# Optimization experiments

Measured on AMD Instinct MI355X. Metric: run time of the kernel, lower is better.

## Reference

```python
import jax, jax.numpy as jnp
import numpy as np

D_MODEL, D_K, D_V, N_HEADS = 1024, 64, 64, 16
B, S = 4, 4096
LN_EPS = 1e-5
NORM_EPS = 1e-12  # torch F.normalize default eps


def setup_inputs() -> dict:
    key = jax.random.key(0)
    ks = jax.random.split(key, 9)
    s = 0.02
    return {
        "x": jax.random.normal(ks[0], (B, S, D_MODEL), dtype=jnp.float32),
        # nn.Linear weights have shape [out, in]
        "W_Q": jax.random.normal(ks[1], (N_HEADS * D_K, D_MODEL), dtype=jnp.float32) * s,
        "W_K": jax.random.normal(ks[2], (N_HEADS * D_K, D_MODEL), dtype=jnp.float32) * s,
        "W_V": jax.random.normal(ks[3], (N_HEADS * D_V, D_MODEL), dtype=jnp.float32) * s,
        "W_g": jax.random.normal(ks[4], (N_HEADS * D_V, D_MODEL), dtype=jnp.float32) * s,
        "W_alpha": jax.random.normal(ks[5], (N_HEADS, D_MODEL), dtype=jnp.float32) * s,
        "W_O": jax.random.normal(ks[6], (D_MODEL, N_HEADS * D_V), dtype=jnp.float32) * s,
        "ln_gamma": jnp.ones((D_MODEL,), dtype=jnp.float32),
        "ln_beta": jnp.zeros((D_MODEL,), dtype=jnp.float32),
    }


def reference(x, W_Q, W_K, W_V, W_g, W_alpha, W_O, ln_gamma, ln_beta):
    # --- input projection chain (unfused variant) ---
    Q_raw = jnp.einsum('bsd,od->bso', x, W_Q)               # [B,S,H*Dk] (unused downstream)
    K_raw = jnp.einsum('bsd,od->bso', x, W_K)               # [B,S,H*Dk]
    V = jnp.einsum('bsd,od->bso', x, W_V)                   # [B,S,H*Dv]
    g_raw = jnp.einsum('bsd,od->bso', x, W_g)               # [B,S,H*Dv]
    alpha_raw = jnp.einsum('bsd,od->bso', x, W_alpha)       # [B,S,H]

    # F.normalize over the full last dim (n_heads*d_k), eps clamp on the norm
    K_norm = K_raw / jnp.maximum(jnp.linalg.norm(K_raw, axis=-1, keepdims=True), NORM_EPS)
    gate = jax.nn.silu(g_raw)
    alpha = jax.nn.sigmoid(alpha_raw)

    # scan is simulated as identity: scan_output = V
    scan_output = V

    # --- output epilogue: gate-multiply + output GEMM + residual + LayerNorm ---
    gated = scan_output * gate
    projected = jnp.einsum('bsv,dv->bsd', gated, W_O)
    pre = projected + x
    mean = jnp.mean(pre, axis=-1, keepdims=True)
    var = jnp.mean(jnp.square(pre - mean), axis=-1, keepdims=True)
    out = (pre - mean) * jax.lax.rsqrt(var + LN_EPS) * ln_gamma + ln_beta
    return out
```

## Files before the change

### kernel.cpp

```cpp
#include <hip/hip_runtime.h>

#define M_TOT 16384
#define DM    1024

typedef unsigned short ushort_t;
typedef __bf16 bf16x8 __attribute__((ext_vector_type(8)));
typedef float  f32x4  __attribute__((ext_vector_type(4)));

__device__ __forceinline__ ushort_t f32_to_bf16(float f) {
    union { float f; unsigned u; } v; v.f = f;
    unsigned u = v.u;
    return (ushort_t)((u + 0x7fffu + ((u >> 16) & 1u)) >> 16);
}
__device__ __forceinline__ float bf16_to_f32(ushort_t h) {
    union { unsigned u; float f; } v; v.u = ((unsigned)h) << 16;
    return v.f;
}

__device__ __forceinline__ void gload16(const ushort_t* g, ushort_t* l) {
    __builtin_amdgcn_global_load_lds(
        (const __attribute__((address_space(1))) unsigned int*)g,
        (__attribute__((address_space(3))) unsigned int*)l,
        16, 0, 0);
}

__global__ __launch_bounds__(256) void cvt_all(const float* __restrict__ x,
                                               const float* __restrict__ wv,
                                               const float* __restrict__ wg,
                                               const float* __restrict__ wo,
                                               ushort_t* __restrict__ xb,
                                               ushort_t* __restrict__ wcat,
                                               ushort_t* __restrict__ wob) {
    const long NX = (long)M_TOT * DM / 4, NW = (long)DM * DM / 4;
    long i = (long)blockIdx.x * 256 + threadIdx.x;
    const float* src; ushort_t* dst; long so, di;
    if (i < NX) {
        src = x; so = i; dst = xb; di = i;
    } else if (i < NX + NW) {
        long j = i - NX; src = wv; so = j;
        int row = (int)(j >> 8), c4 = (int)(j & 255);
        int orow = ((row >> 4) << 5) | (row & 15);
        dst = wcat; di = (long)orow * 256 + c4;
    } else if (i < NX + 2 * NW) {
        long j = i - NX - NW; src = wg; so = j;
        int row = (int)(j >> 8), c4 = (int)(j & 255);
        int orow = ((row >> 4) << 5) | 16 | (row & 15);
        dst = wcat; di = (long)orow * 256 + c4;
    } else {
        long j = i - NX - 2 * NW; src = wo; so = j; dst = wob; di = j;
    }
    const float4 v = ((const float4*)src)[so];
    ushort4 o;
    o.x = f32_to_bf16(v.x); o.y = f32_to_bf16(v.y);
    o.z = f32_to_bf16(v.z); o.w = f32_to_bf16(v.w);
    ((ushort4*)dst)[di] = o;
}

template<int EPI>
__global__ __launch_bounds__(512, 2) void gemmS(
    const ushort_t* __restrict__ A,
    const ushort_t* __restrict__ Bm,
    const ushort_t* __restrict__ Xb,
    ushort_t* __restrict__ out,
    int nbs)
{
    extern __shared__ ushort_t lds[];

    const int flat = blockIdx.x;
    const int xcd  = flat & 7;
    const int ii   = flat >> 3;
    const int m0   = ((xcd << 3) + (ii >> nbs)) << 8;
    const int n0   = (ii & ((1 << nbs) - 1)) << 8;

    const int tid  = threadIdx.x;
    const int w    = tid >> 6;
    const int l    = tid & 63;
    const int wm   = w >> 2;
    const int wn   = w & 3;
    const int fr   = l & 15;
    const int quad = l >> 4;

    f32x4 acc[8][4];
    const f32x4 vzero = {0.f, 0.f, 0.f, 0.f};
#pragma unroll
    for (int i = 0; i < 8; ++i)
#pragma unroll
        for (int j = 0; j < 4; ++j) acc[i][j] = vzero;

    const long sA0 = (long)(m0 + w * 16 + fr) * DM + (quad << 3);
    const long sA1 = sA0 + 128 * (long)DM;
    const long sB0 = (long)(n0 + w * 16 + fr) * DM + (quad << 3);
    const long sB1 = sB0 + 128 * (long)DM;

    auto stageA = [&](int u) {
        const int d  = (u & 3) * 16384 + w * 512;
        const int ko = u * 32;
        gload16(A + sA0 + ko, lds + d);
        gload16(A + sA1 + ko, lds + d + 4096);
    };
    auto stageB = [&](int u) {
        const int d  = (u & 3) * 16384 + 8192 + w * 512;
        const int ko = u * 32;
        gload16(Bm + sB0 + ko, lds + d);
        gload16(Bm + sB1 + ko, lds + d + 4096);
    };

    const int rA = wm * 4096 + l * 8;
    const int rB = 8192 + wn * 2048 + l * 8;

    stageA(0); stageB(0);
    stageA(1); stageB(1);
    stageA(2); stageB(2);
    asm volatile("s_waitcnt vmcnt(8)" ::: "memory");
    __builtin_amdgcn_s_barrier();

    for (int u = 0; u < 32; ++u) {
        const int sb = (u & 3) * 16384;
        bf16x8 af[4], bf[4];

#pragma unroll
        for (int j = 0; j < 4; ++j) bf[j] = *(const bf16x8*)(lds + sb + rB + j * 512);
#pragma unroll
        for (int i = 0; i < 4; ++i) af[i] = *(const bf16x8*)(lds + sb + rA + i * 512);
        if (u < 29) stageA(u + 3);
        __builtin_amdgcn_s_barrier();
        __builtin_amdgcn_s_setprio(1);
#pragma unroll
        for (int j = 0; j < 4; ++j)
#pragma unroll
            for (int i = 0; i < 4; ++i)
                acc[i][j] = __builtin_amdgcn_mfma_f32_16x16x32_bf16(
                    af[i], bf[j], acc[i][j], 0, 0, 0);
        __builtin_amdgcn_s_setprio(0);
        __builtin_amdgcn_s_barrier();

#pragma unroll
        for (int i = 0; i < 4; ++i) af[i] = *(const bf16x8*)(lds + sb + rA + (4 + i) * 512);
        if (u < 29) stageB(u + 3);
        __builtin_amdgcn_s_barrier();
        __builtin_amdgcn_s_setprio(1);
#pragma unroll
        for (int j = 0; j < 4; ++j)
#pragma unroll
            for (int i = 0; i < 4; ++i)
                acc[4 + i][j] = __builtin_amdgcn_mfma_f32_16x16x32_bf16(
                    af[i], bf[j], acc[4 + i][j], 0, 0, 0);
        __builtin_amdgcn_s_setprio(0);
        if (u < 29)       { asm volatile("s_waitcnt vmcnt(8)" ::: "memory"); }
        else if (u == 29) { asm volatile("s_waitcnt vmcnt(4)" ::: "memory"); }
        else if (u == 30) { asm volatile("s_waitcnt vmcnt(0)" ::: "memory"); }
        __builtin_amdgcn_sched_barrier(0);
        __builtin_amdgcn_s_barrier();
    }

    const int rowb = m0 + wm * 128;
    const int colb = n0 + wn * 64;
    if (EPI == 0) {
#pragma unroll
        for (int i = 0; i < 8; ++i)
#pragma unroll
            for (int jp = 0; jp < 2; ++jp) {
                const int cb   = colb + jp * 32;
                const int vcol = ((cb >> 5) << 4) + fr;
#pragma unroll
                for (int r = 0; r < 4; ++r) {
                    const int row = rowb + i * 16 + quad * 4 + r;
                    float v = acc[i][2 * jp][r];
                    float g = acc[i][2 * jp + 1][r];
                    float gate = g / (1.0f + __expf(-g));
                    out[(long)row * DM + vcol] = f32_to_bf16(v * gate);
                }
            }
    } else {
#pragma unroll
        for (int i = 0; i < 8; ++i)
#pragma unroll
            for (int j = 0; j < 4; ++j) {
                const int col = colb + j * 16 + fr;
#pragma unroll
                for (int r = 0; r < 4; ++r) {
                    const int row = rowb + i * 16 + quad * 4 + r;
                    float pre = acc[i][j][r] + bf16_to_f32(Xb[(long)row * DM + col]);
                    out[(long)row * DM + col] = f32_to_bf16(pre);
                }
            }
    }
}

__global__ __launch_bounds__(256) void ln_rows(const ushort_t* __restrict__ pre,
                                               const float* __restrict__ gamma,
                                               const float* __restrict__ beta,
                                               float* __restrict__ out)
{
    const int row = blockIdx.x;
    const int tid = threadIdx.x;
    const int wave = tid >> 6, lane = tid & 63;

    ushort4 u = ((const ushort4*)(pre + row * DM))[tid];
    float p0 = bf16_to_f32(u.x), p1 = bf16_to_f32(u.y);
    float p2 = bf16_to_f32(u.z), p3 = bf16_to_f32(u.w);

    float s  = p0 + p1 + p2 + p3;
    float ss = p0 * p0 + p1 * p1 + p2 * p2 + p3 * p3;
#pragma unroll
    for (int off = 32; off > 0; off >>= 1) {
        s  += __shfl_down(s, off);
        ss += __shfl_down(ss, off);
    }
    __shared__ float red[8];
    __shared__ float mb[2];
    if (lane == 0) { red[wave] = s; red[4 + wave] = ss; }
    __syncthreads();
    if (tid == 0) {
        float S  = red[0] + red[1] + red[2] + red[3];
        float SS = red[4] + red[5] + red[6] + red[7];
        float mean = S * (1.0f / 1024.0f);
        float var  = SS * (1.0f / 1024.0f) - mean * mean;
        mb[0] = mean;
        mb[1] = rsqrtf(var + 1e-5f);
    }
    __syncthreads();
    const float mean = mb[0], rs = mb[1];

    float4 gm = ((const float4*)gamma)[tid];
    float4 bt = ((const float4*)beta)[tid];
    float4 o;
    o.x = (p0 - mean) * rs * gm.x + bt.x;
    o.y = (p1 - mean) * rs * gm.y + bt.y;
    o.z = (p2 - mean) * rs * gm.z + bt.z;
    o.w = (p3 - mean) * rs * gm.w + bt.w;
    ((float4*)(out + row * DM))[tid] = o;
}

extern "C" void kernel_launch(void* const* d_in, const int* in_sizes, int n_in,
                              void* d_out, int out_size, void* d_ws, size_t ws_size,
                              hipStream_t stream) {
    const float* x     = (const float*)d_in[0];
    const float* WV    = (const float*)d_in[3];
    const float* WG    = (const float*)d_in[4];
    const float* WO    = (const float*)d_in[6];
    const float* gamma = (const float*)d_in[7];
    const float* beta  = (const float*)d_in[8];
    float* out = (float*)d_out;

    char* ws = (char*)d_ws;
    ushort_t* xb    = (ushort_t*)ws;
    ushort_t* gated = (ushort_t*)(ws + (size_t)M_TOT * DM * 2);
    ushort_t* wcat  = (ushort_t*)(ws + (size_t)M_TOT * DM * 4);
    ushort_t* wob   = (ushort_t*)(ws + (size_t)M_TOT * DM * 4 + (size_t)2 * DM * DM * 2);
    ushort_t* pre   = xb;

    static bool attr_set = false;
    if (!attr_set) {
        hipFuncSetAttribute((const void*)&gemmS<0>,
                            hipFuncAttributeMaxDynamicSharedMemorySize, 131072);
        hipFuncSetAttribute((const void*)&gemmS<1>,
                            hipFuncAttributeMaxDynamicSharedMemorySize, 131072);
        attr_set = true;
    }

    const int nCvt = (M_TOT * DM + 3 * DM * DM) / 4 / 256;
    cvt_all<<<nCvt, 256, 0, stream>>>(x, WV, WG, WO, xb, wcat, wob);

    gemmS<0><<<512, 512, 131072, stream>>>(xb, wcat, nullptr, gated, 3);
    gemmS<1><<<256, 512, 131072, stream>>>(gated, wob, xb, pre, 2);

    ln_rows<<<M_TOT, 256, 0, stream>>>(pre, gamma, beta, out);
}
```

Before: 270.4 us.

## Split-K the output GEMM into two halves and sum partials in LayerNorm

The output projection GEMM, which launched only 256 blocks, now splits K into two halves. That gives 512 blocks to fill the GPU better. Each half writes its bf16 partial to a separate buffer, and a new LayerNorm kernel adds both partials plus the residual before normalising. The split path is used only when the workspace is large enough. It adds extra global traffic for a second partial buffer and rounds each partial to bf16.

```diff
diff --git a/kernel.cpp b/kernel.cpp
--- a/kernel.cpp
+++ b/kernel.cpp
@@ -56,21 +56,25 @@
     ((ushort4*)dst)[di] = o;
 }
 
-template<int EPI>
+template<int EPI, int NU>
 __global__ __launch_bounds__(512, 2) void gemmS(
     const ushort_t* __restrict__ A,
     const ushort_t* __restrict__ Bm,
     const ushort_t* __restrict__ Xb,
-    ushort_t* __restrict__ out,
+    ushort_t* __restrict__ out0,
+    ushort_t* __restrict__ out1,
     int nbs)
 {
     extern __shared__ ushort_t lds[];
 
     const int flat = blockIdx.x;
     const int xcd  = flat & 7;
-    const int ii   = flat >> 3;
+    int ii = flat >> 3;
+    int kslice = 0;
+    if (EPI == 2) { kslice = ii & 1; ii >>= 1; }
     const int m0   = ((xcd << 3) + (ii >> nbs)) << 8;
     const int n0   = (ii & ((1 << nbs) - 1)) << 8;
+    const int KU0  = (EPI == 2) ? kslice * NU : 0;
 
     const int tid  = threadIdx.x;
     const int w    = tid >> 6;
@@ -87,9 +91,9 @@
 #pragma unroll
         for (int j = 0; j < 4; ++j) acc[i][j] = vzero;
 
-    const long sA0 = (long)(m0 + w * 16 + fr) * DM + (quad << 3);
+    const long sA0 = (long)(m0 + w * 16 + fr) * DM + (quad << 3) + KU0 * 32;
     const long sA1 = sA0 + 128 * (long)DM;
-    const long sB0 = (long)(n0 + w * 16 + fr) * DM + (quad << 3);
+    const long sB0 = (long)(n0 + w * 16 + fr) * DM + (quad << 3) + KU0 * 32;
     const long sB1 = sB0 + 128 * (long)DM;
 
     auto stageA = [&](int u) {
@@ -114,7 +118,7 @@
     asm volatile("s_waitcnt vmcnt(8)" ::: "memory");
     __builtin_amdgcn_s_barrier();
 
-    for (int u = 0; u < 32; ++u) {
+    for (int u = 0; u < NU; ++u) {
         const int sb = (u & 3) * 16384;
         bf16x8 af[4], bf[4];
 
@@ -122,7 +126,7 @@
         for (int j = 0; j < 4; ++j) bf[j] = *(const bf16x8*)(lds + sb + rB + j * 512);
 #pragma unroll
         for (int i = 0; i < 4; ++i) af[i] = *(const bf16x8*)(lds + sb + rA + i * 512);
-        if (u < 29) stageA(u + 3);
+        if (u < NU - 3) stageA(u + 3);
         __builtin_amdgcn_s_barrier();
         __builtin_amdgcn_s_setprio(1);
 #pragma unroll
@@ -136,7 +140,7 @@
 
 #pragma unroll
         for (int i = 0; i < 4; ++i) af[i] = *(const bf16x8*)(lds + sb + rA + (4 + i) * 512);
-        if (u < 29) stageB(u + 3);
+        if (u < NU - 3) stageB(u + 3);
         __builtin_amdgcn_s_barrier();
         __builtin_amdgcn_s_setprio(1);
 #pragma unroll
@@ -146,9 +150,9 @@
                 acc[4 + i][j] = __builtin_amdgcn_mfma_f32_16x16x32_bf16(
                     af[i], bf[j], acc[4 + i][j], 0, 0, 0);
         __builtin_amdgcn_s_setprio(0);
-        if (u < 29)       { asm volatile("s_waitcnt vmcnt(8)" ::: "memory"); }
-        else if (u == 29) { asm volatile("s_waitcnt vmcnt(4)" ::: "memory"); }
-        else if (u == 30) { asm volatile("s_waitcnt vmcnt(0)" ::: "memory"); }
+        if (u < NU - 3)       { asm volatile("s_waitcnt vmcnt(8)" ::: "memory"); }
+        else if (u == NU - 3) { asm volatile("s_waitcnt vmcnt(4)" ::: "memory"); }
+        else if (u == NU - 2) { asm volatile("s_waitcnt vmcnt(0)" ::: "memory"); }
         __builtin_amdgcn_sched_barrier(0);
         __builtin_amdgcn_s_barrier();
     }
@@ -168,10 +172,24 @@
                     float v = acc[i][2 * jp][r];
                     float g = acc[i][2 * jp + 1][r];
                     float gate = g / (1.0f + __expf(-g));
-                    out[(long)row * DM + vcol] = f32_to_bf16(v * gate);
+                    out0[(long)row * DM + vcol] = f32_to_bf16(v * gate);
+                }
+            }
+    } else if (EPI == 1) {
+#pragma unroll
+        for (int i = 0; i < 8; ++i)
+#pragma unroll
+            for (int j = 0; j < 4; ++j) {
+                const int col = colb + j * 16 + fr;
+#pragma unroll
+                for (int r = 0; r < 4; ++r) {
+                    const int row = rowb + i * 16 + quad * 4 + r;
+                    float pre = acc[i][j][r] + bf16_to_f32(Xb[(long)row * DM + col]);
+                    out0[(long)row * DM + col] = f32_to_bf16(pre);
                 }
             }
     } else {
+        ushort_t* po = kslice ? out1 : out0;
 #pragma unroll
         for (int i = 0; i < 8; ++i)
 #pragma unroll
@@ -180,8 +198,7 @@
 #pragma unroll
                 for (int r = 0; r < 4; ++r) {
                     const int row = rowb + i * 16 + quad * 4 + r;
-                    float pre = acc[i][j][r] + bf16_to_f32(Xb[(long)row * DM + col]);
-                    out[(long)row * DM + col] = f32_to_bf16(pre);
+                    po[(long)row * DM + col] = f32_to_bf16(acc[i][j][r]);
                 }
             }
     }
@@ -196,7 +213,7 @@
     const int tid = threadIdx.x;
     const int wave = tid >> 6, lane = tid & 63;
 
-    ushort4 u = ((const ushort4*)(pre + row * DM))[tid];
+    ushort4 u = ((const ushort4*)(pre + (long)row * DM))[tid];
     float p0 = bf16_to_f32(u.x), p1 = bf16_to_f32(u.y);
     float p2 = bf16_to_f32(u.z), p3 = bf16_to_f32(u.w);
 
@@ -229,7 +246,59 @@
     o.y = (p1 - mean) * rs * gm.y + bt.y;
     o.z = (p2 - mean) * rs * gm.z + bt.z;
     o.w = (p3 - mean) * rs * gm.w + bt.w;
-    ((float4*)(out + row * DM))[tid] = o;
+    ((float4*)(out + (long)row * DM))[tid] = o;
+}
+
+__global__ __launch_bounds__(256) void ln_rows3(const ushort_t* __restrict__ pA,
+                                                const ushort_t* __restrict__ pB,
+                                                const ushort_t* __restrict__ xb,
+                                                const float* __restrict__ gamma,
+                                                const float* __restrict__ beta,
+                                                float* __restrict__ out)
+{
+    const int row = blockIdx.x;
+    const int tid = threadIdx.x;
+    const int wave = tid >> 6, lane = tid & 63;
+    const long ro = (long)row * DM;
+
+    ushort4 ua = ((const ushort4*)(pA + ro))[tid];
+    ushort4 ub = ((const ushort4*)(pB + ro))[tid];
+    ushort4 ux = ((const ushort4*)(xb + ro))[tid];
+    float p0 = bf16_to_f32(ua.x) + bf16_to_f32(ub.x) + bf16_to_f32(ux.x);
+    float p1 = bf16_to_f32(ua.y) + bf16_to_f32(ub.y) + bf16_to_f32(ux.y);
+    float p2 = bf16_to_f32(ua.z) + bf16_to_f32(ub.z) + bf16_to_f32(ux.z);
+    float p3 = bf16_to_f32(ua.w) + bf16_to_f32(ub.w) + bf16_to_f32(ux.w);
+
+    float s  = p0 + p1 + p2 + p3;
+    float ss = p0 * p0 + p1 * p1 + p2 * p2 + p3 * p3;
+#pragma unroll
+    for (int off = 32; off > 0; off >>= 1) {
+        s  += __shfl_down(s, off);
+        ss += __shfl_down(ss, off);
+    }
+    __shared__ float red[8];
+    __shared__ float mb[2];
+    if (lane == 0) { red[wave] = s; red[4 + wave] = ss; }
+    __syncthreads();
+    if (tid == 0) {
+        float S  = red[0] + red[1] + red[2] + red[3];
+        float SS = red[4] + red[5] + red[6] + red[7];
+        float mean = S * (1.0f / 1024.0f);
+        float var  = SS * (1.0f / 1024.0f) - mean * mean;
+        mb[0] = mean;
+        mb[1] = rsqrtf(var + 1e-5f);
+    }
+    __syncthreads();
+    const float mean = mb[0], rs = mb[1];
+
+    float4 gm = ((const float4*)gamma)[tid];
+    float4 bt = ((const float4*)beta)[tid];
+    float4 o;
+    o.x = (p0 - mean) * rs * gm.x + bt.x;
+    o.y = (p1 - mean) * rs * gm.y + bt.y;
+    o.z = (p2 - mean) * rs * gm.z + bt.z;
+    o.w = (p3 - mean) * rs * gm.w + bt.w;
+    ((float4*)(out + ro))[tid] = o;
 }
 
 extern "C" void kernel_launch(void* const* d_in, const int* in_sizes, int n_in,
@@ -243,18 +312,24 @@
     const float* beta  = (const float*)d_in[8];
     float* out = (float*)d_out;
 
+    const size_t SZX = (size_t)M_TOT * DM * 2;
+    const size_t SZW = (size_t)DM * DM * 2;
     char* ws = (char*)d_ws;
     ushort_t* xb    = (ushort_t*)ws;
-    ushort_t* gated = (ushort_t*)(ws + (size_t)M_TOT * DM * 2);
-    ushort_t* wcat  = (ushort_t*)(ws + (size_t)M_TOT * DM * 4);
-    ushort_t* wob   = (ushort_t*)(ws + (size_t)M_TOT * DM * 4 + (size_t)2 * DM * DM * 2);
-    ushort_t* pre   = xb;
+    ushort_t* gated = (ushort_t*)(ws + SZX);
+    ushort_t* wcat  = (ushort_t*)(ws + 2 * SZX);
+    ushort_t* wob   = (ushort_t*)(ws + 2 * SZX + 2 * SZW);
+    ushort_t* projA = (ushort_t*)(ws + 2 * SZX + 3 * SZW);
+    ushort_t* projB = (ushort_t*)(ws + 3 * SZX + 3 * SZW);
+    const bool splitk = ws_size >= 4 * SZX + 3 * SZW;
 
     static bool attr_set = false;
     if (!attr_set) {
-        hipFuncSetAttribute((const void*)&gemmS<0>,
+        hipFuncSetAttribute((const void*)&gemmS<0, 32>,
                             hipFuncAttributeMaxDynamicSharedMemorySize, 131072);
-        hipFuncSetAttribute((const void*)&gemmS<1>,
+        hipFuncSetAttribute((const void*)&gemmS<1, 32>,
+                            hipFuncAttributeMaxDynamicSharedMemorySize, 131072);
+        hipFuncSetAttribute((const void*)&gemmS<2, 16>,
                             hipFuncAttributeMaxDynamicSharedMemorySize, 131072);
         attr_set = true;
     }
@@ -262,8 +337,13 @@
     const int nCvt = (M_TOT * DM + 3 * DM * DM) / 4 / 256;
     cvt_all<<<nCvt, 256, 0, stream>>>(x, WV, WG, WO, xb, wcat, wob);
 
-    gemmS<0><<<512, 512, 131072, stream>>>(xb, wcat, nullptr, gated, 3);
-    gemmS<1><<<256, 512, 131072, stream>>>(gated, wob, xb, pre, 2);
-
-    ln_rows<<<M_TOT, 256, 0, stream>>>(pre, gamma, beta, out);
-}
+    gemmS<0, 32><<<512, 512, 131072, stream>>>(xb, wcat, nullptr, gated, nullptr, 3);
+
+    if (splitk) {
+        gemmS<2, 16><<<512, 512, 131072, stream>>>(gated, wob, nullptr, projA, projB, 2);
+        ln_rows3<<<M_TOT, 256, 0, stream>>>(projA, projB, xb, gamma, beta, out);
+    } else {
+        gemmS<1, 32><<<256, 512, 131072, stream>>>(gated, wob, xb, xb, nullptr, 2);
+        ln_rows<<<M_TOT, 256, 0, stream>>>(xb, gamma, beta, out);
+    }
+}
```

After: 286.8 us. 1.06x slower.

## Load GEMM B-operand directly into registers, staging only A through LDS

Applied to the files above, without the earlier changes.

The GEMM kernel now stages only the A tile in LDS, a 4-deep ring of half the previous size. Each wave loads its B fragments straight from global memory into registers, double-buffered across k-steps. This halves LDS traffic and footprint (64KB instead of 128KB) and merges the two half-steps into one 32-MFMA block per barrier. In exchange, B fragments are fetched redundantly by every wave sharing a column slice, and global-load latency for B is exposed with only one step of lookahead.

```diff
diff --git a/kernel.cpp b/kernel.cpp
--- a/kernel.cpp
+++ b/kernel.cpp
@@ -57,7 +57,7 @@
 }
 
 template<int EPI>
-__global__ __launch_bounds__(512, 2) void gemmS(
+__global__ __launch_bounds__(512, 2) void gemmR(
     const ushort_t* __restrict__ A,
     const ushort_t* __restrict__ Bm,
     const ushort_t* __restrict__ Xb,
@@ -87,70 +87,65 @@
 #pragma unroll
         for (int j = 0; j < 4; ++j) acc[i][j] = vzero;
 
-    const long sA0 = (long)(m0 + w * 16 + fr) * DM + (quad << 3);
-    const long sA1 = sA0 + 128 * (long)DM;
-    const long sB0 = (long)(n0 + w * 16 + fr) * DM + (quad << 3);
-    const long sB1 = sB0 + 128 * (long)DM;
-
-    auto stageA = [&](int u) {
-        const int d  = (u & 3) * 16384 + w * 512;
+    const int sA0 = (m0 + w * 16 + fr) * DM + (quad << 3);
+    const int sA1 = sA0 + 128 * DM;
+
+    auto stage = [&](int u) {
+        const int d  = (u & 3) * 8192 + w * 512;
         const int ko = u * 32;
         gload16(A + sA0 + ko, lds + d);
         gload16(A + sA1 + ko, lds + d + 4096);
     };
-    auto stageB = [&](int u) {
-        const int d  = (u & 3) * 16384 + 8192 + w * 512;
+
+    int bOff[4];
+#pragma unroll
+    for (int j = 0; j < 4; ++j)
+        bOff[j] = (n0 + wn * 64 + j * 16 + fr) * DM + (quad << 3);
+
+    const int rA = wm * 4096 + l * 8;
+
+    bf16x8 bf0[4], bf1[4];
+
+    auto loadB = [&](bf16x8 (&dst)[4], int u) {
         const int ko = u * 32;
-        gload16(Bm + sB0 + ko, lds + d);
-        gload16(Bm + sB1 + ko, lds + d + 4096);
+#pragma unroll
+        for (int j = 0; j < 4; ++j)
+            dst[j] = *(const bf16x8*)(Bm + bOff[j] + ko);
     };
 
-    const int rA = wm * 4096 + l * 8;
-    const int rB = 8192 + wn * 2048 + l * 8;
-
-    stageA(0); stageB(0);
-    stageA(1); stageB(1);
-    stageA(2); stageB(2);
-    asm volatile("s_waitcnt vmcnt(8)" ::: "memory");
+    loadB(bf0, 0);
+    stage(0); stage(1); stage(2);
+    asm volatile("s_waitcnt vmcnt(6)" ::: "memory");
     __builtin_amdgcn_s_barrier();
 
-    for (int u = 0; u < 32; ++u) {
-        const int sb = (u & 3) * 16384;
-        bf16x8 af[4], bf[4];
-
-#pragma unroll
-        for (int j = 0; j < 4; ++j) bf[j] = *(const bf16x8*)(lds + sb + rB + j * 512);
-#pragma unroll
-        for (int i = 0; i < 4; ++i) af[i] = *(const bf16x8*)(lds + sb + rA + i * 512);
-        if (u < 29) stageA(u + 3);
-        __builtin_amdgcn_s_barrier();
-        __builtin_amdgcn_s_setprio(1);
-#pragma unroll
-        for (int j = 0; j < 4; ++j)
-#pragma unroll
-            for (int i = 0; i < 4; ++i)
-                acc[i][j] = __builtin_amdgcn_mfma_f32_16x16x32_bf16(
-                    af[i], bf[j], acc[i][j], 0, 0, 0);
-        __builtin_amdgcn_s_setprio(0);
-        __builtin_amdgcn_s_barrier();
-
-#pragma unroll
-        for (int i = 0; i < 4; ++i) af[i] = *(const bf16x8*)(lds + sb + rA + (4 + i) * 512);
-        if (u < 29) stageB(u + 3);
-        __builtin_amdgcn_s_barrier();
-        __builtin_amdgcn_s_setprio(1);
-#pragma unroll
-        for (int j = 0; j < 4; ++j)
-#pragma unroll
-            for (int i = 0; i < 4; ++i)
-                acc[4 + i][j] = __builtin_amdgcn_mfma_f32_16x16x32_bf16(
-                    af[i], bf[j], acc[4 + i][j], 0, 0, 0);
-        __builtin_amdgcn_s_setprio(0);
-        if (u < 29)       { asm volatile("s_waitcnt vmcnt(8)" ::: "memory"); }
-        else if (u == 29) { asm volatile("s_waitcnt vmcnt(4)" ::: "memory"); }
-        else if (u == 30) { asm volatile("s_waitcnt vmcnt(0)" ::: "memory"); }
+    auto unit = [&](int u, bf16x8 (&bfC)[4], bf16x8 (&bfN)[4]) {
+        const int sb = (u & 3) * 8192;
+        bf16x8 af[8];
+#pragma unroll
+        for (int i = 0; i < 8; ++i) af[i] = *(const bf16x8*)(lds + sb + rA + i * 512);
+        if (u < 31) loadB(bfN, u + 1);
+        if (u < 29) stage(u + 3);
         __builtin_amdgcn_sched_barrier(0);
         __builtin_amdgcn_s_barrier();
+
+        __builtin_amdgcn_s_setprio(1);
+#pragma unroll
+        for (int j = 0; j < 4; ++j)
+#pragma unroll
+            for (int i = 0; i < 8; ++i)
+                acc[i][j] = __builtin_amdgcn_mfma_f32_16x16x32_bf16(
+                    af[i], bfC[j], acc[i][j], 0, 0, 0);
+        __builtin_amdgcn_s_setprio(0);
+
+        if (u == 0)       { asm volatile("s_waitcnt vmcnt(8)"  ::: "memory"); }
+        else if (u < 29)  { asm volatile("s_waitcnt vmcnt(12)" ::: "memory"); }
+        else if (u == 29) { asm volatile("s_waitcnt vmcnt(10)" ::: "memory"); }
+        else if (u == 30) { asm volatile("s_waitcnt vmcnt(8)"  ::: "memory"); }
+    };
+
+    for (int t = 0; t < 16; ++t) {
+        unit(2 * t,     bf0, bf1);
+        unit(2 * t + 1, bf1, bf0);
     }
 
     const int rowb = m0 + wm * 128;
@@ -196,7 +191,7 @@
     const int tid = threadIdx.x;
     const int wave = tid >> 6, lane = tid & 63;
 
-    ushort4 u = ((const ushort4*)(pre + row * DM))[tid];
+    ushort4 u = ((const ushort4*)(pre + (long)row * DM))[tid];
     float p0 = bf16_to_f32(u.x), p1 = bf16_to_f32(u.y);
     float p2 = bf16_to_f32(u.z), p3 = bf16_to_f32(u.w);
 
@@ -229,7 +224,7 @@
     o.y = (p1 - mean) * rs * gm.y + bt.y;
     o.z = (p2 - mean) * rs * gm.z + bt.z;
     o.w = (p3 - mean) * rs * gm.w + bt.w;
-    ((float4*)(out + row * DM))[tid] = o;
+    ((float4*)(out + (long)row * DM))[tid] = o;
 }
 
 extern "C" void kernel_launch(void* const* d_in, const int* in_sizes, int n_in,
@@ -243,27 +238,29 @@
     const float* beta  = (const float*)d_in[8];
     float* out = (float*)d_out;
 
+    const size_t SZX = (size_t)M_TOT * DM * 2;
+    const size_t SZW = (size_t)DM * DM * 2;
     char* ws = (char*)d_ws;
     ushort_t* xb    = (ushort_t*)ws;
-    ushort_t* gated = (ushort_t*)(ws + (size_t)M_TOT * DM * 2);
-    ushort_t* wcat  = (ushort_t*)(ws + (size_t)M_TOT * DM * 4);
-    ushort_t* wob   = (ushort_t*)(ws + (size_t)M_TOT * DM * 4 + (size_t)2 * DM * DM * 2);
+    ushort_t* gated = (ushort_t*)(ws + SZX);
+    ushort_t* wcat  = (ushort_t*)(ws + 2 * SZX);
+    ushort_t* wob   = (ushort_t*)(ws + 2 * SZX + 2 * SZW);
     ushort_t* pre   = xb;
 
     static bool attr_set = false;
     if (!attr_set) {
-        hipFuncSetAttribute((const void*)&gemmS<0>,
-                            hipFuncAttributeMaxDynamicSharedMemorySize, 131072);
-        hipFuncSetAttribute((const void*)&gemmS<1>,
-                            hipFuncAttributeMaxDynamicSharedMemorySize, 131072);
+        hipFuncSetAttribute((const void*)&gemmR<0>,
+                            hipFuncAttributeMaxDynamicSharedMemorySize, 65536);
+        hipFuncSetAttribute((const void*)&gemmR<1>,
+                            hipFuncAttributeMaxDynamicSharedMemorySize, 65536);
         attr_set = true;
     }
 
     const int nCvt = (M_TOT * DM + 3 * DM * DM) / 4 / 256;
     cvt_all<<<nCvt, 256, 0, stream>>>(x, WV, WG, WO, xb, wcat, wob);
 
-    gemmS<0><<<512, 512, 131072, stream>>>(xb, wcat, nullptr, gated, 3);
-    gemmS<1><<<256, 512, 131072, stream>>>(gated, wob, xb, pre, 2);
+    gemmR<0><<<512, 512, 65536, stream>>>(xb, wcat, nullptr, gated, 3);
+    gemmR<1><<<256, 512, 65536, stream>>>(gated, wob, xb, pre, 2);
 
     ln_rows<<<M_TOT, 256, 0, stream>>>(pre, gamma, beta, out);
 }
```

New measurement: 310.7 us. 1.15x slower.

## Add warp-specialized producer/consumer GEMM for fused V/gate projection

Applied to the files above, without the earlier changes.

Replaces the first projection GEMM with a warp-specialized kernel in which one dedicated producer wave issues all global-to-LDS loads into a 4-stage ring, and eight consumer waves run MFMAs. Stages are handed off through LDS flag counters rather than block-wide barriers. The aim is to decouple memory loads from math and drop barrier stalls. In exchange, occupancy falls to one block per CU, and the spin-wait flags use relaxed atomics, which risks ordering hazards and idle waits.

```diff
diff --git a/kernel.cpp b/kernel.cpp
--- a/kernel.cpp
+++ b/kernel.cpp
@@ -56,12 +56,141 @@
     ((ushort4*)dst)[di] = o;
 }
 
-template<int EPI>
+__global__ __launch_bounds__(576, 1) void gemmP(
+    const ushort_t* __restrict__ A,
+    const ushort_t* __restrict__ Bm,
+    ushort_t* __restrict__ out,
+    int nbs)
+{
+    extern __shared__ ushort_t lds[];
+    int* flags = (int*)(lds + 65536);
+
+    const int flat = blockIdx.x;
+    const int xcd  = flat & 7;
+    const int ii   = flat >> 3;
+    const int m0   = ((xcd << 3) + (ii >> nbs)) << 8;
+    const int n0   = (ii & ((1 << nbs) - 1)) << 8;
+
+    const int tid  = threadIdx.x;
+    const int w    = tid >> 6;
+    const int l    = tid & 63;
+    const int NU   = 32;
+
+    if (tid < 8) flags[tid] = 0;
+    __syncthreads();
+
+    if (w == 8) {
+        int aBase[16], bBase[16];
+#pragma unroll
+        for (int t = 0; t < 16; ++t) {
+            const int ro = ((t & 7) << 4) + ((t >> 3) << 7) + (l & 15);
+            aBase[t] = (m0 + ro) * DM + ((l >> 4) << 3);
+            bBase[t] = (n0 + ro) * DM + ((l >> 4) << 3);
+        }
+        for (int v = 0; v < NU; ++v) {
+            const int s = v & 3;
+            if (v >= 4) {
+                const int need = (v >> 2) << 3;
+                while (__hip_atomic_load(&flags[4 + s], __ATOMIC_RELAXED,
+                                         __HIP_MEMORY_SCOPE_WORKGROUP) < need)
+                    __builtin_amdgcn_s_sleep(2);
+            }
+            const int ko = v * 32;
+            ushort_t* dst = lds + s * 16384 + l * 8;
+#pragma unroll
+            for (int t = 0; t < 16; ++t)
+                gload16(A + aBase[t] + ko, dst + t * 512);
+#pragma unroll
+            for (int t = 0; t < 16; ++t)
+                gload16(Bm + bBase[t] + ko, dst + 8192 + t * 512);
+            asm volatile("s_waitcnt vmcnt(0)" ::: "memory");
+            __hip_atomic_store(&flags[s], v + 1, __ATOMIC_RELAXED,
+                               __HIP_MEMORY_SCOPE_WORKGROUP);
+        }
+        return;
+    }
+
+    const int wm   = w >> 2;
+    const int wn   = w & 3;
+    const int fr   = l & 15;
+    const int quad = l >> 4;
+
+    f32x4 acc[8][4];
+    const f32x4 vzero = {0.f, 0.f, 0.f, 0.f};
+#pragma unroll
+    for (int i = 0; i < 8; ++i)
+#pragma unroll
+        for (int j = 0; j < 4; ++j) acc[i][j] = vzero;
+
+    const int rA = wm * 4096 + l * 8;
+    const int rB = 8192 + wn * 2048 + l * 8;
+
+    while (__hip_atomic_load(&flags[0], __ATOMIC_RELAXED,
+                             __HIP_MEMORY_SCOPE_WORKGROUP) < 1)
+        __builtin_amdgcn_s_sleep(1);
+    __builtin_amdgcn_sched_barrier(0);
+
+    for (int u = 0; u < NU; ++u) {
+        const int s  = u & 3;
+        const int sb = s * 16384;
+        bf16x8 af[8], bf[4];
+#pragma unroll
+        for (int j = 0; j < 4; ++j) bf[j] = *(const bf16x8*)(lds + sb + rB + j * 512);
+#pragma unroll
+        for (int i = 0; i < 8; ++i) af[i] = *(const bf16x8*)(lds + sb + rA + i * 512);
+        __builtin_amdgcn_sched_barrier(0);
+        __hip_atomic_fetch_add(&flags[4 + s], 1, __ATOMIC_RELAXED,
+                               __HIP_MEMORY_SCOPE_WORKGROUP);
+        int tok = 0x7fffffff;
+        if (u + 1 < NU)
+            tok = __hip_atomic_load(&flags[(u + 1) & 3], __ATOMIC_RELAXED,
+                                    __HIP_MEMORY_SCOPE_WORKGROUP);
+        __builtin_amdgcn_sched_barrier(0);
+
+        __builtin_amdgcn_s_setprio(1);
+#pragma unroll
+        for (int j = 0; j < 4; ++j)
+#pragma unroll
+            for (int i = 0; i < 8; ++i)
+                acc[i][j] = __builtin_amdgcn_mfma_f32_16x16x32_bf16(
+                    af[i], bf[j], acc[i][j], 0, 0, 0);
+        __builtin_amdgcn_s_setprio(0);
+
+        if (u + 1 < NU) {
+            while (tok < u + 2) {
+                __builtin_amdgcn_s_sleep(1);
+                tok = __hip_atomic_load(&flags[(u + 1) & 3], __ATOMIC_RELAXED,
+                                        __HIP_MEMORY_SCOPE_WORKGROUP);
+            }
+            __builtin_amdgcn_sched_barrier(0);
+        }
+    }
+
+    const int rowb = m0 + wm * 128;
+    const int colb = n0 + wn * 64;
+#pragma unroll
+    for (int i = 0; i < 8; ++i)
+#pragma unroll
+        for (int jp = 0; jp < 2; ++jp) {
+            const int cb   = colb + jp * 32;
+            const int vcol = ((cb >> 5) << 4) + fr;
+#pragma unroll
+            for (int r = 0; r < 4; ++r) {
+                const int row = rowb + i * 16 + quad * 4 + r;
+                float v = acc[i][2 * jp][r];
+                float g = acc[i][2 * jp + 1][r];
+                float gate = g / (1.0f + __expf(-g));
+                out[(long)row * DM + vcol] = f32_to_bf16(v * gate);
+            }
+        }
+}
+
+template<int EPI, int NU>
 __global__ __launch_bounds__(512, 2) void gemmS(
     const ushort_t* __restrict__ A,
     const ushort_t* __restrict__ Bm,
     const ushort_t* __restrict__ Xb,
-    ushort_t* __restrict__ out,
+    ushort_t* __restrict__ out0,
     int nbs)
 {
     extern __shared__ ushort_t lds[];
@@ -114,15 +243,14 @@
     asm volatile("s_waitcnt vmcnt(8)" ::: "memory");
     __builtin_amdgcn_s_barrier();
 
-    for (int u = 0; u < 32; ++u) {
+    for (int u = 0; u < NU; ++u) {
         const int sb = (u & 3) * 16384;
         bf16x8 af[4], bf[4];
-
 #pragma unroll
         for (int j = 0; j < 4; ++j) bf[j] = *(const bf16x8*)(lds + sb + rB + j * 512);
 #pragma unroll
         for (int i = 0; i < 4; ++i) af[i] = *(const bf16x8*)(lds + sb + rA + i * 512);
-        if (u < 29) stageA(u + 3);
+        if (u < NU - 3) stageA(u + 3);
         __builtin_amdgcn_s_barrier();
         __builtin_amdgcn_s_setprio(1);
 #pragma unroll
@@ -136,7 +264,7 @@
 
 #pragma unroll
         for (int i = 0; i < 4; ++i) af[i] = *(const bf16x8*)(lds + sb + rA + (4 + i) * 512);
-        if (u < 29) stageB(u + 3);
+        if (u < NU - 3) stageB(u + 3);
         __builtin_amdgcn_s_barrier();
         __builtin_amdgcn_s_setprio(1);
 #pragma unroll
@@ -146,9 +274,9 @@
                 acc[4 + i][j] = __builtin_amdgcn_mfma_f32_16x16x32_bf16(
                     af[i], bf[j], acc[4 + i][j], 0, 0, 0);
         __builtin_amdgcn_s_setprio(0);
-        if (u < 29)       { asm volatile("s_waitcnt vmcnt(8)" ::: "memory"); }
-        else if (u == 29) { asm volatile("s_waitcnt vmcnt(4)" ::: "memory"); }
-        else if (u == 30) { asm volatile("s_waitcnt vmcnt(0)" ::: "memory"); }
+        if (u < NU - 3)       { asm volatile("s_waitcnt vmcnt(8)" ::: "memory"); }
+        else if (u == NU - 3) { asm volatile("s_waitcnt vmcnt(4)" ::: "memory"); }
+        else if (u == NU - 2) { asm volatile("s_waitcnt vmcnt(0)" ::: "memory"); }
         __builtin_amdgcn_sched_barrier(0);
         __builtin_amdgcn_s_barrier();
     }
@@ -168,7 +296,7 @@
                     float v = acc[i][2 * jp][r];
                     float g = acc[i][2 * jp + 1][r];
                     float gate = g / (1.0f + __expf(-g));
-                    out[(long)row * DM + vcol] = f32_to_bf16(v * gate);
+                    out0[(long)row * DM + vcol] = f32_to_bf16(v * gate);
                 }
             }
     } else {
@@ -181,7 +309,7 @@
                 for (int r = 0; r < 4; ++r) {
                     const int row = rowb + i * 16 + quad * 4 + r;
                     float pre = acc[i][j][r] + bf16_to_f32(Xb[(long)row * DM + col]);
-                    out[(long)row * DM + col] = f32_to_bf16(pre);
+                    out0[(long)row * DM + col] = f32_to_bf16(pre);
                 }
             }
     }
@@ -196,7 +324,7 @@
     const int tid = threadIdx.x;
     const int wave = tid >> 6, lane = tid & 63;
 
-    ushort4 u = ((const ushort4*)(pre + row * DM))[tid];
+    ushort4 u = ((const ushort4*)(pre + (long)row * DM))[tid];
     float p0 = bf16_to_f32(u.x), p1 = bf16_to_f32(u.y);
     float p2 = bf16_to_f32(u.z), p3 = bf16_to_f32(u.w);
 
@@ -229,7 +357,7 @@
     o.y = (p1 - mean) * rs * gm.y + bt.y;
     o.z = (p2 - mean) * rs * gm.z + bt.z;
     o.w = (p3 - mean) * rs * gm.w + bt.w;
-    ((float4*)(out + row * DM))[tid] = o;
+    ((float4*)(out + (long)row * DM))[tid] = o;
 }
 
 extern "C" void kernel_launch(void* const* d_in, const int* in_sizes, int n_in,
@@ -243,18 +371,20 @@
     const float* beta  = (const float*)d_in[8];
     float* out = (float*)d_out;
 
+    const size_t SZX = (size_t)M_TOT * DM * 2;
+    const size_t SZW = (size_t)DM * DM * 2;
     char* ws = (char*)d_ws;
     ushort_t* xb    = (ushort_t*)ws;
-    ushort_t* gated = (ushort_t*)(ws + (size_t)M_TOT * DM * 2);
-    ushort_t* wcat  = (ushort_t*)(ws + (size_t)M_TOT * DM * 4);
-    ushort_t* wob   = (ushort_t*)(ws + (size_t)M_TOT * DM * 4 + (size_t)2 * DM * DM * 2);
+    ushort_t* gated = (ushort_t*)(ws + SZX);
+    ushort_t* wcat  = (ushort_t*)(ws + 2 * SZX);
+    ushort_t* wob   = (ushort_t*)(ws + 2 * SZX + 2 * SZW);
     ushort_t* pre   = xb;
 
     static bool attr_set = false;
     if (!attr_set) {
-        hipFuncSetAttribute((const void*)&gemmS<0>,
-                            hipFuncAttributeMaxDynamicSharedMemorySize, 131072);
-        hipFuncSetAttribute((const void*)&gemmS<1>,
+        hipFuncSetAttribute((const void*)&gemmP,
+                            hipFuncAttributeMaxDynamicSharedMemorySize, 131104);
+        hipFuncSetAttribute((const void*)&gemmS<1, 32>,
                             hipFuncAttributeMaxDynamicSharedMemorySize, 131072);
         attr_set = true;
     }
@@ -262,8 +392,8 @@
     const int nCvt = (M_TOT * DM + 3 * DM * DM) / 4 / 256;
     cvt_all<<<nCvt, 256, 0, stream>>>(x, WV, WG, WO, xb, wcat, wob);
 
-    gemmS<0><<<512, 512, 131072, stream>>>(xb, wcat, nullptr, gated, 3);
-    gemmS<1><<<256, 512, 131072, stream>>>(gated, wob, xb, pre, 2);
+    gemmP<<<512, 576, 131104, stream>>>(xb, wcat, gated, 3);
+    gemmS<1, 32><<<256, 512, 131072, stream>>>(gated, wob, xb, pre, 2);
 
     ln_rows<<<M_TOT, 256, 0, stream>>>(pre, gamma, beta, out);
 }
```

After: 373.0 us. +37.9%, slower.
